# Performance work log

Measured on AMD Instinct MI355X. Metric: run time of the kernel, lower is better.

The kernel has to match this reference:

```python
import jax, jax.numpy as jnp
import numpy as np

REG_C = 0.01
REG_THETA_M = 0.01
REG_THETA_P = 0.01
EPS = 1e-20


def setup_inputs() -> dict:
    key = jax.random.key(0)
    k1, k2, k3 = jax.random.split(key, 3)
    B, L, M, P = 128, 16, 32, 4  # batch, num_site, M, P
    input_ds = jax.random.uniform(k1, (B, L), dtype=jnp.float32)
    theta = jax.random.uniform(k2, (L, M, P), dtype=jnp.float32, minval=-1.0, maxval=1.0)
    coef = jax.random.uniform(k3, (M, P), dtype=jnp.float32, minval=-1.0, maxval=1.0)
    return {"input_ds": input_ds, "theta": theta, "coef": coef}


def reference(input_ds, theta, coef):
    # theta: (L, M, P); coef: (M, P); input_ds: (B, L)
    L, M, P = theta.shape
    p_range = jnp.arange(P, dtype=theta.dtype)
    scaling_factor = jnp.pi / 2.0 ** (p_range + 1.0)          # (P,)
    x = scaling_factor[None, None, :] * input_ds[:, :, None]   # (B, L, P)

    # prob term: sum_{m,p} coef[m,p] * prod_l cos(theta[l,m,p] + x[b,l,p])
    theta_x = theta[None, :, :, :] + x[:, :, None, :]          # (B, L, M, P)
    amp = jnp.einsum('bmp,mp->b', jnp.prod(jnp.cos(theta_x), axis=1), coef)
    prob = amp ** 2                                            # (B,)

    # normalization term over the big (B, L, M, M, P, P) broadcast tensor
    d_theta = theta[:, :, None, :, None] - theta[:, None, :, None, :]   # (L, M, M, P, P)
    d_x = x[:, :, None, None, :, None] - x[:, :, None, None, None, :]   # (B, L, 1, 1, P, P)
    cos_prod = jnp.prod(jnp.cos(d_theta[None] + d_x), axis=1)           # (B, M, M, P, P)
    coef_tensor = jnp.einsum('mp,nq->mnpq', coef, coef)                 # (M, M, P, P)
    normalization = jnp.einsum('bmnpq,mnpq->b', cos_prod, coef_tensor)  # (B,)

    prob_norm = prob / normalization

    # regularization (torch.var is unbiased -> ddof=1)
    reg_theta_m = jnp.mean(jnp.var(theta, axis=1, ddof=1))
    reg_theta_p = jnp.mean(jnp.var(theta, axis=2, ddof=1)) if P != 1 else 0.0
    reg_c = jnp.var(coef, ddof=1)

    loss = (jnp.mean(-jnp.log(prob_norm + EPS))
            + REG_C * reg_c
            + REG_THETA_M * reg_theta_m
            + REG_THETA_P * reg_theta_p)
    return loss
```

## Files before the change

### kernel.cpp

```cpp
#include <hip/hip_runtime.h>
#include <math.h>

#define NB 128
#define NL 16
#define NM 32
#define NP 4
#define NMP 128

__global__ __launch_bounds__(512) void per_b_kernel(
    const float* __restrict__ ds, const float* __restrict__ theta,
    const float* __restrict__ coef, float* __restrict__ wnorm,
    float* __restrict__ wamp)
{
    const int b = blockIdx.x >> 1;
    const int h = blockIdx.x & 1;
    const int t = threadIdx.x;

    __shared__ float2 cs[NL][NMP];
    __shared__ float  co[NMP];
    __shared__ float  dsrow[NL];
    __shared__ float  redN[8], redA[8];

    if (t < NL)  dsrow[t] = ds[b * NL + t];
    if (t < NMP) co[t]    = coef[t];
    __syncthreads();

    for (int i = t; i < NL * NMP; i += 512) {
        int l = i >> 7;
        int j = i & (NMP - 1);
        int p = j & 3;
        float sf = (float)M_PI / (float)(2 << p);
        float u  = theta[i] + sf * dsrow[l];
        float ss, cc;
        sincosf(u, &ss, &cc);
        cs[l][j] = make_float2(cc, ss);
    }
    __syncthreads();

    const int j  = t & (NMP - 1);
    const int kq = t >> 7;
    const int k0 = h * 64 + kq * 16;

    float rc[NL], rs[NL];
    #pragma unroll
    for (int l = 0; l < NL; ++l) { float2 v = cs[l][j]; rc[l] = v.x; rs[l] = v.y; }

    const float wj = co[j];

    float amp_part = 0.f;
    if (h == 0 && kq == 0) {
        float pr = wj;
        #pragma unroll
        for (int l = 0; l < NL; ++l) pr *= rc[l];
        amp_part = pr;
    }

    float norm_part = 0.f;
    #pragma unroll 4
    for (int ki = 0; ki < 16; ++ki) {
        int k = k0 + ki;
        float pp = wj * co[k];
        #pragma unroll
        for (int l = 0; l < NL; ++l) {
            float2 v = cs[l][k];
            pp *= fmaf(rc[l], v.x, rs[l] * v.y);
        }
        norm_part += pp;
    }

    #pragma unroll
    for (int off = 32; off > 0; off >>= 1) {
        norm_part += __shfl_xor(norm_part, off);
        amp_part  += __shfl_xor(amp_part,  off);
    }
    const int wid  = t >> 6;
    const int lane = t & 63;
    if (lane == 0) { redN[wid] = norm_part; redA[wid] = amp_part; }
    __syncthreads();
    if (t == 0) {
        float n = 0.f, a = 0.f;
        #pragma unroll
        for (int w = 0; w < 8; ++w) { n += redN[w]; a += redA[w]; }
        wnorm[b * 2 + h] = n;
        if (h == 0) wamp[b] = a;
    }
}

__global__ __launch_bounds__(256) void finalize_kernel(
    const float* __restrict__ wnorm, const float* __restrict__ wamp,
    const float* __restrict__ theta, const float* __restrict__ coef,
    float* __restrict__ out)
{
    const int t = threadIdx.x;
    __shared__ float r1[256], r2[256];
    __shared__ float s_mnl, s_csum, s_csum2, s_vm;

    float mnl = 0.f;
    if (t < NB) {
        float a = wamp[t];
        float n = wnorm[2 * t] + wnorm[2 * t + 1];
        mnl = -logf(a * a / n + 1e-20f);
    }
    r1[t] = mnl;
    float cv = (t < NMP) ? coef[t] : 0.f;
    r2[t] = cv;
    __syncthreads();
    for (int off = 128; off > 0; off >>= 1) {
        if (t < off) { r1[t] += r1[t + off]; r2[t] += r2[t + off]; }
        __syncthreads();
    }
    if (t == 0) { s_mnl = r1[0] / (float)NB; s_csum = r2[0]; }
    __syncthreads();

    r1[t] = cv * cv;
    float vm = 0.f;
    if (t < NL * NP) {
        int l = t >> 2, p = t & 3;
        float sum = 0.f, sum2 = 0.f;
        for (int m = 0; m < NM; ++m) {
            float x = theta[(l * NM + m) * NP + p];
            sum += x; sum2 += x * x;
        }
        vm = (sum2 - sum * sum / (float)NM) / (float)(NM - 1);
    }
    r2[t] = vm;
    __syncthreads();
    for (int off = 128; off > 0; off >>= 1) {
        if (t < off) { r1[t] += r1[t + off]; r2[t] += r2[t + off]; }
        __syncthreads();
    }
    if (t == 0) { s_csum2 = r1[0]; s_vm = r2[0] / (float)(NL * NP); }
    __syncthreads();

    float vp = 0.f;
    for (int i = t; i < NL * NM; i += 256) {
        const float* base = theta + i * NP;
        float sum = 0.f, sum2 = 0.f;
        #pragma unroll
        for (int p = 0; p < NP; ++p) { float x = base[p]; sum += x; sum2 += x * x; }
        vp += (sum2 - sum * sum / (float)NP) / (float)(NP - 1);
    }
    r1[t] = vp;
    __syncthreads();
    for (int off = 128; off > 0; off >>= 1) {
        if (t < off) r1[t] += r1[t + off];
        __syncthreads();
    }
    if (t == 0) {
        float reg_tp = r1[0] / (float)(NL * NM);
        float reg_c  = (s_csum2 - s_csum * s_csum / (float)NMP) / (float)(NMP - 1);
        out[0] = s_mnl + 0.01f * reg_c + 0.01f * s_vm + 0.01f * reg_tp;
    }
}

extern "C" void kernel_launch(void* const* d_in, const int* in_sizes, int n_in,
                              void* d_out, int out_size, void* d_ws, size_t ws_size,
                              hipStream_t stream) {
    const float* ds    = (const float*)d_in[0];
    const float* theta = (const float*)d_in[1];
    const float* coef  = (const float*)d_in[2];
    float* wnorm = (float*)d_ws;
    float* wamp  = (float*)d_ws + 2 * NB;
    float* out   = (float*)d_out;

    per_b_kernel<<<2 * NB, 512, 0, stream>>>(ds, theta, coef, wnorm, wamp);
    finalize_kernel<<<1, 256, 0, stream>>>(wnorm, wamp, theta, coef, out);
}
```

Measured before the change: 15.15 us.

## Fuse finalize into main kernel via last-block counter, retile norm loop

Merges the finalize step into the main kernel: each block bumps an atomic counter, and the last block to finish performs the loss and regularization reductions using warp shuffles. The norm loop now gives each thread two j columns and eight k values, so every shared-memory load of cs[l][k] feeds two products. It also switches to the fast intrinsics __sincosf and __logf. A hipMemsetAsync is added to reset the counter, which may partly offset the launch removed, and the fast intrinsics reduce accuracy.

```diff
diff --git a/kernel.cpp b/kernel.cpp
--- a/kernel.cpp
+++ b/kernel.cpp
@@ -6,20 +6,26 @@
 #define NM 32
 #define NP 4
 #define NMP 128
+#define GRID (2 * NB)
 
-__global__ __launch_bounds__(512) void per_b_kernel(
+__global__ __launch_bounds__(512) void fused_kernel(
     const float* __restrict__ ds, const float* __restrict__ theta,
     const float* __restrict__ coef, float* __restrict__ wnorm,
-    float* __restrict__ wamp)
+    float* __restrict__ wamp, unsigned int* __restrict__ counter,
+    float* __restrict__ out)
 {
-    const int b = blockIdx.x >> 1;
-    const int h = blockIdx.x & 1;
-    const int t = threadIdx.x;
+    const int b    = blockIdx.x >> 1;
+    const int h    = blockIdx.x & 1;
+    const int t    = threadIdx.x;
+    const int lane = t & 63;
+    const int w    = t >> 6;
 
     __shared__ float2 cs[NL][NMP];
     __shared__ float  co[NMP];
     __shared__ float  dsrow[NL];
     __shared__ float  redN[8], redA[8];
+    __shared__ float  r5[5][8];
+    __shared__ bool   s_last;
 
     if (t < NL)  dsrow[t] = ds[b * NL + t];
     if (t < NMP) co[t]    = coef[t];
@@ -32,40 +38,40 @@
         float sf = (float)M_PI / (float)(2 << p);
         float u  = theta[i] + sf * dsrow[l];
         float ss, cc;
-        sincosf(u, &ss, &cc);
+        __sincosf(u, &ss, &cc);
         cs[l][j] = make_float2(cc, ss);
     }
     __syncthreads();
 
-    const int j  = t & (NMP - 1);
-    const int kq = t >> 7;
-    const int k0 = h * 64 + kq * 16;
-
-    float rc[NL], rs[NL];
+    float rc0[NL], rs0[NL], rc1[NL], rs1[NL];
     #pragma unroll
-    for (int l = 0; l < NL; ++l) { float2 v = cs[l][j]; rc[l] = v.x; rs[l] = v.y; }
-
-    const float wj = co[j];
+    for (int l = 0; l < NL; ++l) {
+        float2 v0 = cs[l][lane];      rc0[l] = v0.x; rs0[l] = v0.y;
+        float2 v1 = cs[l][lane + 64]; rc1[l] = v1.x; rs1[l] = v1.y;
+    }
+    const float wj0 = co[lane], wj1 = co[lane + 64];
 
     float amp_part = 0.f;
-    if (h == 0 && kq == 0) {
-        float pr = wj;
+    if (w == 0) {
+        float p0 = wj0, p1 = wj1;
         #pragma unroll
-        for (int l = 0; l < NL; ++l) pr *= rc[l];
-        amp_part = pr;
+        for (int l = 0; l < NL; ++l) { p0 *= rc0[l]; p1 *= rc1[l]; }
+        amp_part = p0 + p1;
     }
 
     float norm_part = 0.f;
+    const int k0 = h * 64 + w * 8;
     #pragma unroll 4
-    for (int ki = 0; ki < 16; ++ki) {
+    for (int ki = 0; ki < 8; ++ki) {
         int k = k0 + ki;
-        float pp = wj * co[k];
+        float pp0 = 1.f, pp1 = 1.f;
         #pragma unroll
         for (int l = 0; l < NL; ++l) {
             float2 v = cs[l][k];
-            pp *= fmaf(rc[l], v.x, rs[l] * v.y);
+            pp0 *= fmaf(rc0[l], v.x, rs0[l] * v.y);
+            pp1 *= fmaf(rc1[l], v.x, rs1[l] * v.y);
         }
-        norm_part += pp;
+        norm_part = fmaf(fmaf(wj1, pp1, wj0 * pp0), co[k], norm_part);
     }
 
     #pragma unroll
@@ -73,46 +79,32 @@
         norm_part += __shfl_xor(norm_part, off);
         amp_part  += __shfl_xor(amp_part,  off);
     }
-    const int wid  = t >> 6;
-    const int lane = t & 63;
-    if (lane == 0) { redN[wid] = norm_part; redA[wid] = amp_part; }
+    if (lane == 0) { redN[w] = norm_part; redA[w] = amp_part; }
     __syncthreads();
     if (t == 0) {
         float n = 0.f, a = 0.f;
         #pragma unroll
-        for (int w = 0; w < 8; ++w) { n += redN[w]; a += redA[w]; }
+        for (int i = 0; i < 8; ++i) { n += redN[i]; a += redA[i]; }
         wnorm[b * 2 + h] = n;
         if (h == 0) wamp[b] = a;
+        __threadfence();
+        unsigned int old = atomicAdd(counter, 1u);
+        s_last = (old == GRID - 1);
     }
-}
+    __syncthreads();
+    if (!s_last) return;
 
-__global__ __launch_bounds__(256) void finalize_kernel(
-    const float* __restrict__ wnorm, const float* __restrict__ wamp,
-    const float* __restrict__ theta, const float* __restrict__ coef,
-    float* __restrict__ out)
-{
-    const int t = threadIdx.x;
-    __shared__ float r1[256], r2[256];
-    __shared__ float s_mnl, s_csum, s_csum2, s_vm;
+    volatile const float* vn = wnorm;
+    volatile const float* va = wamp;
 
     float mnl = 0.f;
     if (t < NB) {
-        float a = wamp[t];
-        float n = wnorm[2 * t] + wnorm[2 * t + 1];
-        mnl = -logf(a * a / n + 1e-20f);
+        float a = va[t];
+        float n = vn[2 * t] + vn[2 * t + 1];
+        mnl = -__logf(a * a / n + 1e-20f);
     }
-    r1[t] = mnl;
-    float cv = (t < NMP) ? coef[t] : 0.f;
-    r2[t] = cv;
-    __syncthreads();
-    for (int off = 128; off > 0; off >>= 1) {
-        if (t < off) { r1[t] += r1[t + off]; r2[t] += r2[t + off]; }
-        __syncthreads();
-    }
-    if (t == 0) { s_mnl = r1[0] / (float)NB; s_csum = r2[0]; }
-    __syncthreads();
+    float cv = (t < NMP) ? co[t] : 0.f;
 
-    r1[t] = cv * cv;
     float vm = 0.f;
     if (t < NL * NP) {
         int l = t >> 2, p = t & 3;
@@ -123,33 +115,38 @@
         }
         vm = (sum2 - sum * sum / (float)NM) / (float)(NM - 1);
     }
-    r2[t] = vm;
+
+    float4 th = reinterpret_cast<const float4*>(theta)[t];
+    float sum  = th.x + th.y + th.z + th.w;
+    float sum2 = th.x * th.x + th.y * th.y + th.z * th.z + th.w * th.w;
+    float vp = (sum2 - sum * sum * 0.25f) * (1.f / 3.f);
+
+    float v1 = mnl, v2 = cv, v3 = cv * cv, v4 = vm, v5 = vp;
+    #pragma unroll
+    for (int off = 32; off > 0; off >>= 1) {
+        v1 += __shfl_xor(v1, off);
+        v2 += __shfl_xor(v2, off);
+        v3 += __shfl_xor(v3, off);
+        v4 += __shfl_xor(v4, off);
+        v5 += __shfl_xor(v5, off);
+    }
+    if (lane == 0) {
+        r5[0][w] = v1; r5[1][w] = v2; r5[2][w] = v3; r5[3][w] = v4; r5[4][w] = v5;
+    }
     __syncthreads();
-    for (int off = 128; off > 0; off >>= 1) {
-        if (t < off) { r1[t] += r1[t + off]; r2[t] += r2[t + off]; }
-        __syncthreads();
-    }
-    if (t == 0) { s_csum2 = r1[0]; s_vm = r2[0] / (float)(NL * NP); }
-    __syncthreads();
-
-    float vp = 0.f;
-    for (int i = t; i < NL * NM; i += 256) {
-        const float* base = theta + i * NP;
-        float sum = 0.f, sum2 = 0.f;
+    if (t == 0) {
+        float s1 = 0.f, s2 = 0.f, s3 = 0.f, s4 = 0.f, s5 = 0.f;
         #pragma unroll
-        for (int p = 0; p < NP; ++p) { float x = base[p]; sum += x; sum2 += x * x; }
-        vp += (sum2 - sum * sum / (float)NP) / (float)(NP - 1);
-    }
-    r1[t] = vp;
-    __syncthreads();
-    for (int off = 128; off > 0; off >>= 1) {
-        if (t < off) r1[t] += r1[t + off];
-        __syncthreads();
-    }
-    if (t == 0) {
-        float reg_tp = r1[0] / (float)(NL * NM);
-        float reg_c  = (s_csum2 - s_csum * s_csum / (float)NMP) / (float)(NMP - 1);
-        out[0] = s_mnl + 0.01f * reg_c + 0.01f * s_vm + 0.01f * reg_tp;
+        for (int i = 0; i < 8; ++i) {
+            s1 += r5[0][i]; s2 += r5[1][i]; s3 += r5[2][i];
+            s4 += r5[3][i]; s5 += r5[4][i];
+        }
+        float s_mnl   = s1 / (float)NB;
+        float reg_c   = (s3 - s2 * s2 / (float)NMP) / (float)(NMP - 1);
+        float reg_tm  = s4 / (float)(NL * NP);
+        float reg_tp  = s5 / (float)(NL * NM);
+        out[0] = s_mnl + 0.01f * (reg_c + reg_tm + reg_tp);
+        *counter = 0;
     }
 }
 
@@ -161,8 +158,9 @@
     const float* coef  = (const float*)d_in[2];
     float* wnorm = (float*)d_ws;
     float* wamp  = (float*)d_ws + 2 * NB;
+    unsigned int* counter = (unsigned int*)((float*)d_ws + 3 * NB);
     float* out   = (float*)d_out;
 
-    per_b_kernel<<<2 * NB, 512, 0, stream>>>(ds, theta, coef, wnorm, wamp);
-    finalize_kernel<<<1, 256, 0, stream>>>(wnorm, wamp, theta, coef, out);
+    hipMemsetAsync(counter, 0, sizeof(unsigned int), stream);
+    fused_kernel<<<GRID, 512, 0, stream>>>(ds, theta, coef, wnorm, wamp, counter, out);
 }
```

New measurement: 22.36 us. 1.48x slower.
